# Optimization experiments

Measured on AMD Instinct MI355X. Metric: run time of the kernel, lower is better.

Reference implementation:

```python
import jax, jax.numpy as jnp
import numpy as np

N_NODES = 50000
N_EDGES = 800000
IN_DIM = 128
NUM_HEADS = 8
OUT_DIM = 16  # per-head dim; NUM_HEADS*OUT_DIM == IN_DIM


def setup_inputs() -> dict:
    key = jax.random.key(0)
    ks = jax.random.split(key, 9)
    s = 1.0 / np.sqrt(IN_DIM)
    return {
        "h": jax.random.normal(ks[0], (N_NODES, IN_DIM), dtype=jnp.float32),
        "src": jax.random.randint(ks[1], (N_EDGES,), 0, N_NODES),
        "dst": jax.random.randint(ks[2], (N_EDGES,), 0, N_NODES),
        "WQ": jax.random.normal(ks[3], (IN_DIM, NUM_HEADS * OUT_DIM), dtype=jnp.float32) * s,
        "bQ": jnp.zeros((NUM_HEADS * OUT_DIM,), dtype=jnp.float32),
        "WK": jax.random.normal(ks[4], (IN_DIM, NUM_HEADS * OUT_DIM), dtype=jnp.float32) * s,
        "bK": jnp.zeros((NUM_HEADS * OUT_DIM,), dtype=jnp.float32),
        "WV": jax.random.normal(ks[5], (IN_DIM, NUM_HEADS * OUT_DIM), dtype=jnp.float32) * s,
        "bV": jnp.zeros((NUM_HEADS * OUT_DIM,), dtype=jnp.float32),
    }


def reference(h, src, dst, WQ, bQ, WK, bK, WV, bV):
    N = h.shape[0]
    # node projections -> [N, H, D]
    Q = (h @ WQ + bQ).reshape(N, NUM_HEADS, OUT_DIM)
    K = (h @ WK + bK).reshape(N, NUM_HEADS, OUT_DIM)
    V = (h @ WV + bV).reshape(N, NUM_HEADS, OUT_DIM)
    # edge-wise score: (K_src * Q_dst) summed over D, scaled by sqrt(D)
    inv_scale = 1.0 / np.sqrt(OUT_DIM)
    score = jnp.einsum("ehd,ehd->eh", K[src], Q[dst]) * inv_scale  # [E, H]
    score_soft = jnp.exp(jnp.clip(score, -5.0, 5.0))[..., None]    # [E, H, 1]
    # scatter-sum messages to destination nodes
    wV = jax.ops.segment_sum(V[src] * score_soft, dst, num_segments=N)  # [N, H, D]
    z = jax.ops.segment_sum(score_soft, dst, num_segments=N)            # [N, H, 1]
    return wV / (z + 1e-6)
```

## Files before the change

### kernel.cpp

```cpp
#include <hip/hip_runtime.h>
#include <hip/hip_bf16.h>

#define IN_DIM 128
#define NUM_HEADS 8
#define OUT_DIM 16

#define BKT_SHIFT 7
#define BKT_MASK 127
#define NB_MAX 512
#define SB_MAX 512
#define SLAB_SHIFT 13

typedef unsigned int uint;
typedef unsigned short ushort;
using short8 = __attribute__((ext_vector_type(8))) short;
using f32x4  = __attribute__((ext_vector_type(4))) float;
using u32x2  = __attribute__((ext_vector_type(2))) uint;

__device__ inline uint cvt_pk_bf16(float a, float b) {
    uint r;
    asm("v_cvt_pk_bf16_f32 %0, %1, %2" : "=v"(r) : "v"(a), "v"(b));
    return r;
}

__global__ __launch_bounds__(256) void prep_kernel(const float* __restrict__ WQ,
                                                   const float* __restrict__ WK,
                                                   const float* __restrict__ WV,
                                                   ushort* __restrict__ WT) {
    const int t = threadIdx.x;
    int tid = blockIdx.x * 256 + t;
    int n = tid >> 4;
    int kg = tid & 15;
    const float* W = (n < 128) ? WQ : (n < 256) ? WK : WV;
    int c = n & 127;
    union { short8 s; uint u[4]; } o;
    #pragma unroll
    for (int j = 0; j < 4; ++j) {
        float v0 = W[(kg * 8 + 2 * j) * 128 + c];
        float v1 = W[(kg * 8 + 2 * j + 1) * 128 + c];
        o.u[j] = cvt_pk_bf16(v0, v1);
    }
    *(short8*)(WT + (size_t)n * 128 + kg * 8) = o.s;
}

__global__ __launch_bounds__(256) void stage_count(const int* __restrict__ dst,
                                                   int* __restrict__ cntMat,
                                                   int nEdges, int nb) {
    __shared__ int cnt[NB_MAX];
    const int t = threadIdx.x;
    const int blk = blockIdx.x;
    for (int i = t; i < NB_MAX; i += 256) cnt[i] = 0;
    __syncthreads();

    const int e0 = blk * 2048;
    #pragma unroll
    for (int i = 0; i < 2; ++i) {
        int e = e0 + (i * 256 + t) * 4;
        if (e + 3 < nEdges) {
            int4 d4 = *(const int4*)(dst + e);
            atomicAdd(&cnt[d4.x >> BKT_SHIFT], 1);
            atomicAdd(&cnt[d4.y >> BKT_SHIFT], 1);
            atomicAdd(&cnt[d4.z >> BKT_SHIFT], 1);
            atomicAdd(&cnt[d4.w >> BKT_SHIFT], 1);
        } else {
            for (int ee = e; ee < nEdges; ++ee) atomicAdd(&cnt[dst[ee] >> BKT_SHIFT], 1);
        }
    }
    __syncthreads();
    for (int bb = t; bb < nb; bb += 256)
        cntMat[(size_t)blk * NB_MAX + bb] = cnt[bb];
}

__global__ __launch_bounds__(256) void bucket_base(const int* __restrict__ cntMat,
                                                   int* __restrict__ baseMat,
                                                   int* __restrict__ bucketTotal,
                                                   int sb) {
    __shared__ int wsum[4];
    const int bkt = blockIdx.x;
    const int t = threadIdx.x;
    const int lane = t & 63;
    const int wv = t >> 6;

    int c0 = (2 * t     < sb) ? cntMat[(size_t)(2 * t)     * NB_MAX + bkt] : 0;
    int c1 = (2 * t + 1 < sb) ? cntMat[(size_t)(2 * t + 1) * NB_MAX + bkt] : 0;
    int s = c0 + c1;
    int x = s;
    #pragma unroll
    for (int off = 1; off < 64; off <<= 1) { int y = __shfl_up(x, off); if (lane >= off) x += y; }
    if (lane == 63) wsum[wv] = x;
    __syncthreads();
    if (t == 0) {
        int a = 0;
        #pragma unroll
        for (int w = 0; w < 4; ++w) { int tmp = wsum[w]; wsum[w] = a; a += tmp; }
    }
    __syncthreads();
    int prefix = wsum[wv] + (x - s);

    if (2 * t < sb)     baseMat[(size_t)bkt * SB_MAX + 2 * t]     = prefix;
    if (2 * t + 1 < sb) baseMat[(size_t)bkt * SB_MAX + 2 * t + 1] = prefix + c0;
    if (t == 255) bucketTotal[bkt] = prefix + s;
}

__global__ __launch_bounds__(256) void stage_scatter(const int* __restrict__ src,
                                                     const int* __restrict__ dst,
                                                     const int* __restrict__ baseMat,
                                                     uint* __restrict__ slab,
                                                     int nEdges, int nb) {
    __shared__ int base[NB_MAX];
    __shared__ int cur[NB_MAX];
    const int t = threadIdx.x;
    const int blk = blockIdx.x;

    for (int bb = t; bb < nb; bb += 256) {
        base[bb] = baseMat[(size_t)bb * SB_MAX + blk];
        cur[bb] = 0;
    }
    __syncthreads();

    const int e0 = blk * 2048;
    int myDst[8], mySrc[8];
    #pragma unroll
    for (int i = 0; i < 2; ++i) {
        int e = e0 + (i * 256 + t) * 4;
        if (e + 3 < nEdges) {
            int4 d4 = *(const int4*)(dst + e);
            int4 s4 = *(const int4*)(src + e);
            myDst[4*i+0] = d4.x; myDst[4*i+1] = d4.y; myDst[4*i+2] = d4.z; myDst[4*i+3] = d4.w;
            mySrc[4*i+0] = s4.x; mySrc[4*i+1] = s4.y; mySrc[4*i+2] = s4.z; mySrc[4*i+3] = s4.w;
        } else {
            #pragma unroll
            for (int k = 0; k < 4; ++k) {
                int ee = e + k;
                myDst[4*i+k] = (ee < nEdges) ? dst[ee] : -1;
                mySrc[4*i+k] = (ee < nEdges) ? src[ee] : 0;
            }
        }
    }

    #pragma unroll
    for (int i = 0; i < 8; ++i) {
        int d = myDst[i];
        if (d >= 0) {
            int b = d >> BKT_SHIFT;
            int r = atomicAdd(&cur[b], 1);
            slab[((size_t)b << SLAB_SHIFT) + base[b] + r] = (uint)mySrc[i] | ((uint)(d & BKT_MASK) << 17);
        }
    }
}

__global__ __launch_bounds__(64, 2) void sort_proj(const uint* __restrict__ slab,
                                                   const int* __restrict__ bucketTotal,
                                                   int* __restrict__ offsets,
                                                   int* __restrict__ srcSorted,
                                                   const float* __restrict__ h,
                                                   const short* __restrict__ WT,
                                                   const float* __restrict__ bQ,
                                                   const float* __restrict__ bK,
                                                   const float* __restrict__ bV,
                                                   uint* __restrict__ Qout,
                                                   uint* __restrict__ KVout,
                                                   int nNodes, int nEdges, int nb) {
    const int t = threadIdx.x;

    if ((int)blockIdx.x < nb) {
        __shared__ int cnt[128];
        __shared__ int sOutBase;
        const int b = blockIdx.x;
        const int count = bucketTotal[b];
        const uint* rec = slab + ((size_t)b << SLAB_SHIFT);

        int acc = 0;
        for (int i = t; i < b; i += 64) acc += bucketTotal[i];
        #pragma unroll
        for (int off = 32; off; off >>= 1) acc += __shfl_down(acc, off);
        if (t == 0) sOutBase = acc;
        cnt[t] = 0; cnt[t + 64] = 0;
        __syncthreads();

        for (int i = t; i < count; i += 64)
            atomicAdd(&cnt[rec[i] >> 17], 1);
        __syncthreads();

        const int outBase = sOutBase;
        int c0 = cnt[2 * t], c1 = cnt[2 * t + 1];
        int s = c0 + c1;
        int x = s;
        #pragma unroll
        for (int off = 1; off < 64; off <<= 1) { int y = __shfl_up(x, off); if (t >= off) x += y; }
        int prefix = x - s;
        int node0 = b << BKT_SHIFT;
        int g0 = node0 + 2 * t, g1 = node0 + 2 * t + 1;
        if (g0 < nNodes) offsets[g0] = outBase + prefix;
        if (g1 < nNodes) offsets[g1] = outBase + prefix + c0;
        __syncthreads();
        cnt[2 * t] = prefix;
        cnt[2 * t + 1] = prefix + c0;
        __syncthreads();

        for (int i = t; i < count; i += 64) {
            uint r = rec[i];
            int pos = atomicAdd(&cnt[r >> 17], 1);
            srcSorted[outBase + pos] = (int)(r & 0x1ffff);
        }
        if (b == 0 && t == 0) offsets[nNodes] = nEdges;
        return;
    }

    const int gw = blockIdx.x - nb;
    const int lane = t;
    const int lr = lane & 15;
    const int q = lane >> 4;
    const int node0 = (gw >> 1) * 64;
    const int chalf = gw & 1;

    short8 a[4][4];
    #pragma unroll
    for (int g = 0; g < 4; ++g) {
        const int row = node0 + g * 16 + lr;
        const bool ok = row < nNodes;
        #pragma unroll
        for (int ks = 0; ks < 4; ++ks) {
            union { short8 s; uint u[4]; } v;
            if (ok) {
                const float* p = h + (size_t)row * 128 + (ks * 4 + q) * 8;
                float4 f0 = *(const float4*)p;
                float4 f1 = *(const float4*)(p + 4);
                v.u[0] = cvt_pk_bf16(f0.x, f0.y);
                v.u[1] = cvt_pk_bf16(f0.z, f0.w);
                v.u[2] = cvt_pk_bf16(f1.x, f1.y);
                v.u[3] = cvt_pk_bf16(f1.z, f1.w);
            } else {
                v.s = (short8)0;
            }
            a[g][ks] = v.s;
        }
    }

    const short8* WT8 = (const short8*)WT;

    #pragma unroll 1
    for (int cc = 0; cc < 4; ++cc) {
        const int c = chalf * 4 + cc;
        const int nq = c * 16 + lr;
        f32x4 aQ[4] = {{0,0,0,0},{0,0,0,0},{0,0,0,0},{0,0,0,0}};
        f32x4 aK[4] = {{0,0,0,0},{0,0,0,0},{0,0,0,0},{0,0,0,0}};
        f32x4 aV[4] = {{0,0,0,0},{0,0,0,0},{0,0,0,0},{0,0,0,0}};
        #pragma unroll
        for (int ks = 0; ks < 4; ++ks) {
            short8 bq = WT8[(size_t)nq * 16 + ks * 4 + q];
            short8 bk = WT8[(size_t)(nq + 128) * 16 + ks * 4 + q];
            short8 bv = WT8[(size_t)(nq + 256) * 16 + ks * 4 + q];
            #pragma unroll
            for (int g = 0; g < 4; ++g) {
                aQ[g] = __builtin_amdgcn_mfma_f32_16x16x32_bf16(a[g][ks], bq, aQ[g], 0, 0, 0);
                aK[g] = __builtin_amdgcn_mfma_f32_16x16x32_bf16(a[g][ks], bk, aK[g], 0, 0, 0);
                aV[g] = __builtin_amdgcn_mfma_f32_16x16x32_bf16(a[g][ks], bv, aV[g], 0, 0, 0);
            }
        }
        const float biasq = bQ[nq];
        const float biask = bK[nq];
        const float biasv = bV[nq];
        #pragma unroll
        for (int g = 0; g < 4; ++g) {
            #pragma unroll
            for (int r = 0; r < 4; ++r) {
                int node = node0 + g * 16 + q * 4 + r;
                float qval = aQ[g][r] + biasq;
                float qpart = __shfl_xor(qval, 1);
                if (node < nNodes) {
                    if ((lr & 1) == 0)
                        Qout[(size_t)node * 64 + (nq >> 1)] = cvt_pk_bf16(qval, qpart);
                    KVout[(size_t)node * 128 + nq] = cvt_pk_bf16(aK[g][r] + biask, aV[g][r] + biasv);
                }
            }
        }
    }
}

__global__ __launch_bounds__(256) void agg_kernel(const int* __restrict__ offsets,
                                                  const int* __restrict__ srcSorted,
                                                  const uint* __restrict__ Q,
                                                  const uint4* __restrict__ KV,
                                                  float* __restrict__ out,
                                                  int nNodes) {
    int wid = (int)((blockIdx.x * (size_t)blockDim.x + threadIdx.x) >> 6);
    if (wid >= nNodes) return;
    const int lane = threadIdx.x & 63;
    const int li = lane & 31;
    const int hf = lane >> 5;
    const int beg = offsets[wid];
    const int end = offsets[wid + 1];

    u32x2 qp = __builtin_nontemporal_load((const u32x2*)(Q + (size_t)wid * 64) + li);
    f32x4 qv;
    qv.x = __uint_as_float(qp.x << 16);
    qv.y = __uint_as_float(qp.x & 0xffff0000u);
    qv.z = __uint_as_float(qp.y << 16);
    qv.w = __uint_as_float(qp.y & 0xffff0000u);

    f32x4 acc = {0.f, 0.f, 0.f, 0.f};
    float zacc = 0.f;

    auto compute = [&](uint4 u, float mask) {
        float k0 = __uint_as_float(u.x << 16), v0 = __uint_as_float(u.x & 0xffff0000u);
        float k1 = __uint_as_float(u.y << 16), v1 = __uint_as_float(u.y & 0xffff0000u);
        float k2 = __uint_as_float(u.z << 16), v2 = __uint_as_float(u.z & 0xffff0000u);
        float k3 = __uint_as_float(u.w << 16), v3 = __uint_as_float(u.w & 0xffff0000u);
        float p = k0 * qv.x + k1 * qv.y + k2 * qv.z + k3 * qv.w;
        p += __shfl_xor(p, 1);
        p += __shfl_xor(p, 2);
        float e = __expf(fminf(fmaxf(p * 0.25f, -5.0f), 5.0f)) * mask;
        acc.x += v0 * e; acc.y += v1 * e; acc.z += v2 * e; acc.w += v3 * e;
        zacc += e;
    };

    int j = beg;
    for (; j + 8 <= end; j += 8) {
        int sI[4];
        #pragma unroll
        for (int i = 0; i < 4; ++i) sI[i] = __builtin_nontemporal_load(srcSorted + j + 2 * i + hf);
        uint4 u[4];
        #pragma unroll
        for (int i = 0; i < 4; ++i) u[i] = KV[(size_t)sI[i] * 32 + li];
        #pragma unroll
        for (int i = 0; i < 4; ++i) compute(u[i], 1.f);
    }
    for (; j + 2 <= end; j += 2) {
        uint4 u = KV[(size_t)srcSorted[j + hf] * 32 + li];
        compute(u, 1.f);
    }
    if (j < end) {
        uint4 u = KV[(size_t)srcSorted[j] * 32 + li];
        compute(u, hf ? 0.f : 1.f);
    }

    acc.x += __shfl_xor(acc.x, 32);
    acc.y += __shfl_xor(acc.y, 32);
    acc.z += __shfl_xor(acc.z, 32);
    acc.w += __shfl_xor(acc.w, 32);
    zacc  += __shfl_xor(zacc, 32);

    if (hf == 0) {
        float inv = 1.0f / (zacc + 1e-6f);
        f32x4 o = {acc.x * inv, acc.y * inv, acc.z * inv, acc.w * inv};
        __builtin_nontemporal_store(o, (f32x4*)(out + (size_t)wid * 128) + li);
    }
}

extern "C" void kernel_launch(void* const* d_in, const int* in_sizes, int n_in,
                              void* d_out, int out_size, void* d_ws, size_t ws_size,
                              hipStream_t stream) {
    const float* h   = (const float*)d_in[0];
    const int*   src = (const int*)d_in[1];
    const int*   dst = (const int*)d_in[2];
    const float* WQ  = (const float*)d_in[3];
    const float* bQ  = (const float*)d_in[4];
    const float* WK  = (const float*)d_in[5];
    const float* bK  = (const float*)d_in[6];
    const float* WV  = (const float*)d_in[7];
    const float* bV  = (const float*)d_in[8];

    const int nNodes = in_sizes[0] / IN_DIM;
    const int nEdges = in_sizes[1];
    const int nb = (nNodes + (1 << BKT_SHIFT) - 1) >> BKT_SHIFT;
    const int sb = (nEdges + 2047) / 2048;

    float* out = (float*)d_out;
    const size_t nf = (size_t)nNodes * 128;

    uint*   Qw         = (uint*)d_ws;
    uint*   KVw        = Qw + (size_t)nNodes * 64;
    ushort* WTw        = (ushort*)(KVw + nf);
    int*    bucketTotal= (int*)(WTw + 384 * 128);
    int*    offsets    = bucketTotal + NB_MAX;
    int*    srcSorted  = offsets + (nNodes + 1);
    uint*   slab       = (uint*)(srcSorted + nEdges);
    int*    cntMat     = (int*)(slab + ((size_t)NB_MAX << SLAB_SHIFT));
    int*    baseMat    = cntMat + (size_t)SB_MAX * NB_MAX;

    prep_kernel<<<24, 256, 0, stream>>>(WQ, WK, WV, WTw);

    stage_count<<<sb, 256, 0, stream>>>(dst, cntMat, nEdges, nb);
    bucket_base<<<nb, 256, 0, stream>>>(cntMat, baseMat, bucketTotal, sb);
    stage_scatter<<<sb, 256, 0, stream>>>(src, dst, baseMat, slab, nEdges, nb);

    int projWaves = ((nNodes + 63) / 64) * 2;
    sort_proj<<<nb + projWaves, 64, 0, stream>>>(slab, bucketTotal, offsets, srcSorted,
                                                 h, (const short*)WTw, bQ, bK, bV,
                                                 Qw, KVw, nNodes, nEdges, nb);

    int aggBlocks = (nNodes * 64 + 255) / 256;
    agg_kernel<<<aggBlocks, 256, 0, stream>>>(offsets, srcSorted, Qw, (const uint4*)KVw, out, nNodes);
}
```

Baseline: 118.1 us.

## Fuse weight prep into count kernel, software-pipeline agg gathers, tune unroll/occupancy

Merges the weight-transpose prep kernel into the edge-count kernel as extra blocks, saving one launch. The aggregation kernel's main loop is software-pipelined so the next batch of source indices and KV gathers is issued before the current batch is computed, hiding gather latency. It also sets agg_kernel launch bounds to 8 waves per SIMD and unrolls the projection column loop by 2. These add register pressure, and the occupancy hint could cause spills.

Measured after the change: 150.7 us. 27.6% more time.

```diff
diff --git a/kernel.cpp b/kernel.cpp
--- a/kernel.cpp
+++ b/kernel.cpp
@@ -23,31 +23,33 @@
     return r;
 }
 
-__global__ __launch_bounds__(256) void prep_kernel(const float* __restrict__ WQ,
-                                                   const float* __restrict__ WK,
-                                                   const float* __restrict__ WV,
-                                                   ushort* __restrict__ WT) {
+__global__ __launch_bounds__(256) void count_prep(const int* __restrict__ dst,
+                                                  int* __restrict__ cntMat,
+                                                  const float* __restrict__ WQ,
+                                                  const float* __restrict__ WK,
+                                                  const float* __restrict__ WV,
+                                                  ushort* __restrict__ WT,
+                                                  int nEdges, int nb, int sb) {
     const int t = threadIdx.x;
-    int tid = blockIdx.x * 256 + t;
-    int n = tid >> 4;
-    int kg = tid & 15;
-    const float* W = (n < 128) ? WQ : (n < 256) ? WK : WV;
-    int c = n & 127;
-    union { short8 s; uint u[4]; } o;
-    #pragma unroll
-    for (int j = 0; j < 4; ++j) {
-        float v0 = W[(kg * 8 + 2 * j) * 128 + c];
-        float v1 = W[(kg * 8 + 2 * j + 1) * 128 + c];
-        o.u[j] = cvt_pk_bf16(v0, v1);
-    }
-    *(short8*)(WT + (size_t)n * 128 + kg * 8) = o.s;
-}
-
-__global__ __launch_bounds__(256) void stage_count(const int* __restrict__ dst,
-                                                   int* __restrict__ cntMat,
-                                                   int nEdges, int nb) {
+
+    if ((int)blockIdx.x >= sb) {
+        int tid = (blockIdx.x - sb) * 256 + t;
+        int n = tid >> 4;
+        int kg = tid & 15;
+        const float* W = (n < 128) ? WQ : (n < 256) ? WK : WV;
+        int c = n & 127;
+        union { short8 s; uint u[4]; } o;
+        #pragma unroll
+        for (int j = 0; j < 4; ++j) {
+            float v0 = W[(kg * 8 + 2 * j) * 128 + c];
+            float v1 = W[(kg * 8 + 2 * j + 1) * 128 + c];
+            o.u[j] = cvt_pk_bf16(v0, v1);
+        }
+        *(short8*)(WT + (size_t)n * 128 + kg * 8) = o.s;
+        return;
+    }
+
     __shared__ int cnt[NB_MAX];
-    const int t = threadIdx.x;
     const int blk = blockIdx.x;
     for (int i = t; i < NB_MAX; i += 256) cnt[i] = 0;
     __syncthreads();
@@ -239,7 +241,7 @@
 
     const short8* WT8 = (const short8*)WT;
 
-    #pragma unroll 1
+    #pragma unroll 2
     for (int cc = 0; cc < 4; ++cc) {
         const int c = chalf * 4 + cc;
         const int nq = c * 16 + lr;
@@ -278,12 +280,12 @@
     }
 }
 
-__global__ __launch_bounds__(256) void agg_kernel(const int* __restrict__ offsets,
-                                                  const int* __restrict__ srcSorted,
-                                                  const uint* __restrict__ Q,
-                                                  const uint4* __restrict__ KV,
-                                                  float* __restrict__ out,
-                                                  int nNodes) {
+__global__ __launch_bounds__(256, 8) void agg_kernel(const int* __restrict__ offsets,
+                                                     const int* __restrict__ srcSorted,
+                                                     const uint* __restrict__ Q,
+                                                     const uint4* __restrict__ KV,
+                                                     float* __restrict__ out,
+                                                     int nNodes) {
     int wid = (int)((blockIdx.x * (size_t)blockDim.x + threadIdx.x) >> 6);
     if (wid >= nNodes) return;
     const int lane = threadIdx.x & 63;
@@ -316,15 +318,38 @@
     };
 
     int j = beg;
-    for (; j + 8 <= end; j += 8) {
-        int sI[4];
-        #pragma unroll
-        for (int i = 0; i < 4; ++i) sI[i] = __builtin_nontemporal_load(srcSorted + j + 2 * i + hf);
+    const int nFull = (end - beg) >> 3;
+    if (nFull > 0) {
+        int sB[4] = {0, 0, 0, 0};
         uint4 u[4];
-        #pragma unroll
-        for (int i = 0; i < 4; ++i) u[i] = KV[(size_t)sI[i] * 32 + li];
+        {
+            int sA[4];
+            #pragma unroll
+            for (int i = 0; i < 4; ++i) sA[i] = __builtin_nontemporal_load(srcSorted + j + 2 * i + hf);
+            #pragma unroll
+            for (int i = 0; i < 4; ++i) u[i] = KV[(size_t)sA[i] * 32 + li];
+        }
+        if (nFull > 1) {
+            #pragma unroll
+            for (int i = 0; i < 4; ++i) sB[i] = __builtin_nontemporal_load(srcSorted + j + 8 + 2 * i + hf);
+        }
+        for (int b = 0; b + 1 < nFull; ++b, j += 8) {
+            uint4 uN[4];
+            #pragma unroll
+            for (int i = 0; i < 4; ++i) uN[i] = KV[(size_t)sB[i] * 32 + li];
+            int sC[4] = {0, 0, 0, 0};
+            if (b + 2 < nFull) {
+                #pragma unroll
+                for (int i = 0; i < 4; ++i) sC[i] = __builtin_nontemporal_load(srcSorted + j + 16 + 2 * i + hf);
+            }
+            #pragma unroll
+            for (int i = 0; i < 4; ++i) compute(u[i], 1.f);
+            #pragma unroll
+            for (int i = 0; i < 4; ++i) { u[i] = uN[i]; sB[i] = sC[i]; }
+        }
         #pragma unroll
         for (int i = 0; i < 4; ++i) compute(u[i], 1.f);
+        j += 8;
     }
     for (; j + 2 <= end; j += 2) {
         uint4 u = KV[(size_t)srcSorted[j + hf] * 32 + li];
@@ -379,9 +404,8 @@
     int*    cntMat     = (int*)(slab + ((size_t)NB_MAX << SLAB_SHIFT));
     int*    baseMat    = cntMat + (size_t)SB_MAX * NB_MAX;
 
-    prep_kernel<<<24, 256, 0, stream>>>(WQ, WK, WV, WTw);
-
-    stage_count<<<sb, 256, 0, stream>>>(dst, cntMat, nEdges, nb);
+    count_prep<<<sb + 24, 256, 0, stream>>>(dst, cntMat, WQ, WK, WV, WTw, nEdges, nb, sb);
+
     bucket_base<<<nb, 256, 0, stream>>>(cntMat, baseMat, bucketTotal, sb);
     stage_scatter<<<sb, 256, 0, stream>>>(src, dst, baseMat, slab, nEdges, nb);
 
```
